# Kernel optimization log

Measured on AMD Instinct MI355X. Metric: run time of the kernel, lower is better.

The kernel has to match this reference:

```python
import jax, jax.numpy as jnp
import numpy as np
from jax import lax
from functools import partial

MAX_FRAMES = 12
NUM_SAMPLES = 500
SIGMA = 0.05
TOPK = 49
LN_EPS = 1e-5


def perturbed_topk_indicators(scores, noise, k):
    """scores: (b, d), noise: (b, ns, d) -> indicators (b, k, d).
    Equivalent to one_hot(sorted_topk_indices).mean(samples) without
    materializing the (b, ns, k, d) one-hot tensor (histogram scatter)."""
    b, ns, d = noise.shape
    perturbed = scores[:, None, :] + SIGMA * noise          # (b, ns, d)
    _, idx = lax.top_k(perturbed, k)                        # (b, ns, k)
    idx = jnp.sort(idx, axis=-1)                            # ascending, as in torch code
    # scatter-add counts into (b, k, d)
    flat = (jnp.arange(b)[:, None, None] * k + jnp.arange(k)[None, None, :]) * d + idx
    counts = jnp.zeros(b * k * d, scores.dtype).at[flat.ravel()].add(1.0)
    return counts.reshape(b, k, d) / ns


def reference(x, ln_w, ln_b, w_in, w_out1, w_out2):
    B, L, D = x.shape
    N = L // MAX_FRAMES
    xf = x.reshape(B * MAX_FRAMES, N, D)                    # (Bf, N, D)
    Bf = B * MAX_FRAMES

    # ---- STPredictorConv ----
    mu = xf.mean(-1, keepdims=True)
    var = jnp.var(xf, axis=-1, keepdims=True)
    xn = (xf - mu) * lax.rsqrt(var + LN_EPS) * ln_w + ln_b
    h = jax.nn.gelu(jnp.einsum('bnd,cd->bnc', xn, w_in), approximate=False)  # (Bf, N, C=256)
    C = h.shape[-1]
    g = h[:, :1, :].reshape(B, MAX_FRAMES, 1, C).mean(axis=1, keepdims=True)  # (B,1,1,C)
    g = jnp.broadcast_to(g, (B, MAX_FRAMES, 1, C)).reshape(Bf, 1, C)
    cat = jnp.concatenate([h, jnp.broadcast_to(g, (Bf, N, C))], axis=-1)      # (Bf, N, 2C)
    s = jax.nn.gelu(jnp.einsum('bnd,cd->bnc', cat, w_out1), approximate=False)
    s = jnp.einsum('bnc,oc->bno', s, w_out2)                # (Bf, N, 1)
    score = jax.nn.softmax(s, axis=-1)[..., 0]              # softmax over size-1 dim -> ones; faithful

    # ---- perturbed top-k selection over spatial tokens ----
    spatial_score = score[:, 1:]                            # (Bf, N-1)
    noise = jax.random.normal(jax.random.key(42), (Bf, NUM_SAMPLES, N - 1), x.dtype)
    ind = perturbed_topk_indicators(spatial_score, noise, TOPK)  # (Bf, k, N-1)

    cls_feat = xf[:, :1, :]
    spatial_feat = xf[:, 1:, :]
    selected = jnp.einsum('bkl,bld->bkd', ind, spatial_feat)
    out = jnp.concatenate([cls_feat, selected], axis=1)     # (Bf, 1+k, D)
    return out.reshape(B, MAX_FRAMES * (1 + TOPK), D)


def setup_inputs() -> dict:
    key = jax.random.key(0)
    ks = jax.random.split(key, 4)
    B, N, D, C = 8, 197, 512, 256
    x = jax.random.normal(ks[0], (B, MAX_FRAMES * N, D), jnp.float32)
    return {
        'x': x,
        'ln_w': jnp.ones((D,), jnp.float32),
        'ln_b': jnp.zeros((D,), jnp.float32),
        'w_in': jax.random.normal(ks[1], (C, D), jnp.float32) * 0.02,
        'w_out1': jax.random.normal(ks[2], (C, D), jnp.float32) * 0.02,
        'w_out2': jax.random.normal(ks[3], (1, C), jnp.float32) * 0.02,
    }
```

## Files before the change

kernel.cpp:

```cpp
#include <hip/hip_runtime.h>
#include <stdint.h>

constexpr int BF   = 96;
constexpr int NS   = 500;
constexpr int DSP  = 196;
constexpr int KSEL = 49;
constexpr int NTOK = 197;
constexpr int DIM  = 512;
constexpr int ROWSTRIDE = 64;

__device__ __forceinline__ uint32_t rotl32(uint32_t x, int r) {
  return __builtin_amdgcn_alignbit(x, x, 32 - r);
}

__device__ __forceinline__ void threefry2x32(uint32_t x0, uint32_t x1,
                                             uint32_t& o0, uint32_t& o1) {
  const uint32_t ks0 = 0u, ks1 = 42u, ks2 = 0u ^ 42u ^ 0x1BD11BDAu;
  x0 += ks0; x1 += ks1;
#define TF_R(r) { x0 += x1; x1 = rotl32(x1, (r)); x1 ^= x0; }
  TF_R(13) TF_R(15) TF_R(26) TF_R(6)   x0 += ks1; x1 += ks2 + 1u;
  TF_R(17) TF_R(29) TF_R(16) TF_R(24)  x0 += ks2; x1 += ks0 + 2u;
  TF_R(13) TF_R(15) TF_R(26) TF_R(6)   x0 += ks0; x1 += ks1 + 3u;
  TF_R(17) TF_R(29) TF_R(16) TF_R(24)  x0 += ks1; x1 += ks2 + 4u;
  TF_R(13) TF_R(15) TF_R(26) TF_R(6)   x0 += ks2; x1 += ks0 + 5u;
#undef TF_R
  o0 = x0; o1 = x1;
}

__device__ __forceinline__ uint32_t noise_bits(uint32_t p) {
  uint32_t o0, o1;
  threefry2x32(0u, p, o0, o1);
  return o0 ^ o1;
}

__global__ __launch_bounds__(256)
void topk_idx_kernel(uint8_t* __restrict__ idxbuf) {
  const int lane = threadIdx.x & 63;
  const int wid  = (blockIdx.x << 2) | (threadIdx.x >> 6);
  const uint32_t rowbase = (uint32_t)wid * (uint32_t)DSP;

  uint32_t m[4];
#pragma unroll
  for (int g = 0; g < 4; ++g) {
    const int j = (g << 6) | lane;
    uint32_t v = 0u;
    if (j < DSP) v = noise_bits(rowbase + (uint32_t)j) >> 9;
    m[g] = v;
  }

  uint32_t T = 0u;
#pragma unroll 1
  for (int bit = 22; bit >= 0; --bit) {
    const uint32_t cand = T | (1u << bit);
    const int c = __popcll(__ballot(m[0] >= cand))
                + __popcll(__ballot(m[1] >= cand))
                + __popcll(__ballot(m[2] >= cand))
                + __popcll(__ballot(m[3] >= cand));
    if (c >= KSEL) T = cand;
  }

  uint64_t gt[4], eq[4];
#pragma unroll
  for (int g = 0; g < 4; ++g) {
    gt[g] = __ballot(m[g] > T);
    eq[g] = __ballot(m[g] == T);
  }
  eq[3] &= 0xFull;

  const int ngt = __popcll(gt[0]) + __popcll(gt[1]) + __popcll(gt[2]) + __popcll(gt[3]);
  const int need = KSEL - ngt;
  const int e0 = __popcll(eq[0]), e1 = __popcll(eq[1]), e2 = __popcll(eq[2]);
  const uint64_t below = (1ull << lane) - 1ull;

  uint64_t fin[4];
  fin[0] = gt[0] | __ballot(((eq[0] >> lane) & 1ull) &&
                            (__popcll(eq[0] & below) < need));
  fin[1] = gt[1] | __ballot(((eq[1] >> lane) & 1ull) &&
                            (e0 + __popcll(eq[1] & below) < need));
  fin[2] = gt[2] | __ballot(((eq[2] >> lane) & 1ull) &&
                            (e0 + e1 + __popcll(eq[2] & below) < need));
  fin[3] = gt[3] | __ballot(((eq[3] >> lane) & 1ull) &&
                            (e0 + e1 + e2 + __popcll(eq[3] & below) < need));

  const int c0 = __popcll(fin[0]);
  const int c1 = c0 + __popcll(fin[1]);
  const int c2 = c1 + __popcll(fin[2]);

  uint8_t* row = idxbuf + (size_t)wid * ROWSTRIDE;
  if ((fin[0] >> lane) & 1ull) row[__popcll(fin[0] & below)]      = (uint8_t)lane;
  if ((fin[1] >> lane) & 1ull) row[c0 + __popcll(fin[1] & below)] = (uint8_t)(64 + lane);
  if ((fin[2] >> lane) & 1ull) row[c1 + __popcll(fin[2] & below)] = (uint8_t)(128 + lane);
  if ((fin[3] >> lane) & 1ull) row[c2 + __popcll(fin[3] & below)] = (uint8_t)(192 + lane);
}

__global__ __launch_bounds__(256)
void hist_kernel(const uint8_t* __restrict__ idxbuf,
                 uint16_t* __restrict__ cnt) {
  const int b = blockIdx.x % BF;
  const int g = blockIdx.x / BF;
  const int t = threadIdx.x;

  __shared__ uint32_t hist[8 * DSP];
  for (int i = t; i < 8 * DSP; i += 256) hist[i] = 0u;
  __syncthreads();

  const uint8_t* base = idxbuf + (size_t)b * NS * ROWSTRIDE + 8 * g;
  for (int r = t; r < NS; r += 256) {
    const uint2 v = *(const uint2*)(base + (size_t)r * ROWSTRIDE);
#pragma unroll
    for (int q = 0; q < 2; ++q) {
      uint32_t w = q ? v.y : v.x;
#pragma unroll
      for (int bb = 0; bb < 4; ++bb) {
        atomicAdd(&hist[(q * 4 + bb) * DSP + (w & 0xffu)], 1u);
        w >>= 8;
      }
    }
  }
  __syncthreads();

  uint16_t* cb = cnt + (size_t)b * KSEL * DSP;
  for (int i = t; i < 8 * DSP; i += 256) {
    const int rank = 8 * g + i / DSP;
    if (rank < KSEL) cb[(size_t)rank * DSP + (i % DSP)] = (uint16_t)hist[i];
  }
}

__global__ __launch_bounds__(256)
void gemm_kernel(const float* __restrict__ x,
                 const uint16_t* __restrict__ cnt,
                 float* __restrict__ out) {
  const int b = blockIdx.x % BF;
  const int tmp = blockIdx.x / BF;
  const int dtile = tmp & 7;
  const int khalf = tmp >> 3;
  const int k0 = khalf * 24;
  const int t = threadIdx.x;
  const int dt = t & 15, kg = t >> 4;

  constexpr int JP = DSP / 2;
  __shared__ uint32_t cfp[32 * JP];
  const uint32_t* cp = (const uint32_t*)(cnt + (size_t)b * KSEL * DSP)
                     + (size_t)k0 * JP;
  for (int i = t; i < 25 * JP; i += 256) cfp[i] = cp[i];
  for (int i = 25 * JP + t; i < 32 * JP; i += 256) cfp[i] = 0u;
  __syncthreads();

  const float* xb = x + (size_t)b * NTOK * DIM + DIM
                  + dtile * 64 + dt * 4;
  float4 acc[2] = {};
#pragma unroll 2
  for (int j2 = 0; j2 < JP; ++j2) {
    const float4 xv0 = *(const float4*)(xb + (size_t)(2 * j2) * DIM);
    const float4 xv1 = *(const float4*)(xb + (size_t)(2 * j2 + 1) * DIM);
#pragma unroll
    for (int i = 0; i < 2; ++i) {
      const uint32_t pr = cfp[(kg + 16 * i) * JP + j2];
      const float c0 = (float)(pr & 0xffffu);
      const float c1 = (float)(pr >> 16);
      acc[i].x = fmaf(c0, xv0.x, acc[i].x);
      acc[i].y = fmaf(c0, xv0.y, acc[i].y);
      acc[i].z = fmaf(c0, xv0.z, acc[i].z);
      acc[i].w = fmaf(c0, xv0.w, acc[i].w);
      acc[i].x = fmaf(c1, xv1.x, acc[i].x);
      acc[i].y = fmaf(c1, xv1.y, acc[i].y);
      acc[i].z = fmaf(c1, xv1.z, acc[i].z);
      acc[i].w = fmaf(c1, xv1.w, acc[i].w);
    }
  }

  float* ob = out + (size_t)b * (1 + KSEL) * DIM + dtile * 64 + dt * 4;
  const float inv = 1.0f / (float)NS;
#pragma unroll
  for (int i = 0; i < 2; ++i) {
    const int kl = kg + 16 * i;
    const int k = k0 + kl;
    if (kl < 25 && k < KSEL) {
      float4 r;
      r.x = acc[i].x * inv; r.y = acc[i].y * inv;
      r.z = acc[i].z * inv; r.w = acc[i].w * inv;
      *(float4*)(ob + (size_t)(1 + k) * DIM) = r;
    }
  }

  if (khalf == 0 && kg == 0) {
    const float4 c4 = *(const float4*)(x + (size_t)b * NTOK * DIM
                                       + dtile * 64 + dt * 4);
    *(float4*)(ob) = c4;
  }
}

extern "C" void kernel_launch(void* const* d_in, const int* in_sizes, int n_in,
                              void* d_out, int out_size, void* d_ws, size_t ws_size,
                              hipStream_t stream) {
  const float* x = (const float*)d_in[0];
  float* out = (float*)d_out;
  uint8_t* idxbuf = (uint8_t*)d_ws;
  uint16_t* cnt = (uint16_t*)((uint8_t*)d_ws +
                              (size_t)BF * NS * ROWSTRIDE);

  topk_idx_kernel<<<dim3(BF * NS / 4), 256, 0, stream>>>(idxbuf);
  hist_kernel<<<dim3(BF * 7), 256, 0, stream>>>(idxbuf, cnt);
  gemm_kernel<<<dim3(BF * 8 * 2), 256, 0, stream>>>(x, cnt, out);
}
```

Baseline: 165.5 us.

## Stage x tiles in LDS and compute all 49 ranks per block in gemm

The gemm kernel no longer splits the 49 ranks into two halves. Each block now computes all ranks for one 64-column tile, which halves the grid and stops x being read twice. Counts are converted to float once into padded shared memory. x is staged through a 32-row LDS tile, with the next tile's global loads issued while the current one is consumed. This adds register pressure, larger LDS use, and a syncthreads-bound loop, and the 49th rank runs on only one thread group.

```diff
diff --git a/kernel.cpp b/kernel.cpp
--- a/kernel.cpp
+++ b/kernel.cpp
@@ -131,59 +131,107 @@
                  const uint16_t* __restrict__ cnt,
                  float* __restrict__ out) {
   const int b = blockIdx.x % BF;
-  const int tmp = blockIdx.x / BF;
-  const int dtile = tmp & 7;
-  const int khalf = tmp >> 3;
-  const int k0 = khalf * 24;
+  const int dtile = blockIdx.x / BF;
   const int t = threadIdx.x;
   const int dt = t & 15, kg = t >> 4;
 
-  constexpr int JP = DSP / 2;
-  __shared__ uint32_t cfp[32 * JP];
-  const uint32_t* cp = (const uint32_t*)(cnt + (size_t)b * KSEL * DSP)
-                     + (size_t)k0 * JP;
-  for (int i = t; i < 25 * JP; i += 256) cfp[i] = cp[i];
-  for (int i = 25 * JP + t; i < 32 * JP; i += 256) cfp[i] = 0u;
-  __syncthreads();
-
-  const float* xb = x + (size_t)b * NTOK * DIM + DIM
-                  + dtile * 64 + dt * 4;
-  float4 acc[2] = {};
-#pragma unroll 2
-  for (int j2 = 0; j2 < JP; ++j2) {
-    const float4 xv0 = *(const float4*)(xb + (size_t)(2 * j2) * DIM);
-    const float4 xv1 = *(const float4*)(xb + (size_t)(2 * j2 + 1) * DIM);
-#pragma unroll
-    for (int i = 0; i < 2; ++i) {
-      const uint32_t pr = cfp[(kg + 16 * i) * JP + j2];
-      const float c0 = (float)(pr & 0xffffu);
-      const float c1 = (float)(pr >> 16);
-      acc[i].x = fmaf(c0, xv0.x, acc[i].x);
-      acc[i].y = fmaf(c0, xv0.y, acc[i].y);
-      acc[i].z = fmaf(c0, xv0.z, acc[i].z);
-      acc[i].w = fmaf(c0, xv0.w, acc[i].w);
-      acc[i].x = fmaf(c1, xv1.x, acc[i].x);
-      acc[i].y = fmaf(c1, xv1.y, acc[i].y);
-      acc[i].z = fmaf(c1, xv1.z, acc[i].z);
-      acc[i].w = fmaf(c1, xv1.w, acc[i].w);
+  constexpr int CFS = 225;
+  __shared__ float cf[KSEL * CFS];
+  __shared__ float xl[32 * 64];
+
+  const uint32_t* cp = (const uint32_t*)(cnt + (size_t)b * KSEL * DSP);
+  for (int i = t; i < KSEL * (DSP / 2); i += 256) {
+    const uint32_t v = cp[i];
+    const int r = i / (DSP / 2), q = i % (DSP / 2);
+    cf[r * CFS + 2 * q]     = (float)(v & 0xffffu);
+    cf[r * CFS + 2 * q + 1] = (float)(v >> 16);
+  }
+  for (int i = t; i < KSEL * (CFS - DSP); i += 256) {
+    const int r = i / (CFS - DSP), q = i % (CFS - DSP);
+    cf[r * CFS + DSP + q] = 0.0f;
+  }
+
+  const float* xsrc = x + (size_t)b * NTOK * DIM + DIM + dtile * 64;
+  const int jl = t >> 3;
+  const int cl = (t & 7) * 8;
+
+  float4 p0, p1;
+  {
+    const float* s = xsrc + (size_t)jl * DIM + cl;
+    p0 = *(const float4*)(s);
+    p1 = *(const float4*)(s + 4);
+  }
+
+  float4 acc[4] = {};
+#pragma unroll 1
+  for (int c = 0; c < 7; ++c) {
+    __syncthreads();
+    {
+      float* d = &xl[jl * 64 + cl];
+      *(float4*)(d) = p0;
+      *(float4*)(d + 4) = p1;
+    }
+    __syncthreads();
+    if (c < 6) {
+      const int nj = 32 * (c + 1);
+      if (c + 1 < 6 || jl < 4) {
+        const float* s = xsrc + (size_t)(nj + jl) * DIM + cl;
+        p0 = *(const float4*)(s);
+        p1 = *(const float4*)(s + 4);
+      }
+    }
+    const int jb = 32 * c;
+#pragma unroll 4
+    for (int j = 0; j < 32; ++j) {
+      const float4 xv = *(const float4*)&xl[j * 64 + dt * 4];
+      const int jc = jb + j;
+      {
+        const float cv = cf[kg * CFS + jc];
+        acc[0].x = fmaf(cv, xv.x, acc[0].x);
+        acc[0].y = fmaf(cv, xv.y, acc[0].y);
+        acc[0].z = fmaf(cv, xv.z, acc[0].z);
+        acc[0].w = fmaf(cv, xv.w, acc[0].w);
+      }
+      {
+        const float cv = cf[(kg + 16) * CFS + jc];
+        acc[1].x = fmaf(cv, xv.x, acc[1].x);
+        acc[1].y = fmaf(cv, xv.y, acc[1].y);
+        acc[1].z = fmaf(cv, xv.z, acc[1].z);
+        acc[1].w = fmaf(cv, xv.w, acc[1].w);
+      }
+      {
+        const float cv = cf[(kg + 32) * CFS + jc];
+        acc[2].x = fmaf(cv, xv.x, acc[2].x);
+        acc[2].y = fmaf(cv, xv.y, acc[2].y);
+        acc[2].z = fmaf(cv, xv.z, acc[2].z);
+        acc[2].w = fmaf(cv, xv.w, acc[2].w);
+      }
+      if (kg == 0) {
+        const float cv = cf[48 * CFS + jc];
+        acc[3].x = fmaf(cv, xv.x, acc[3].x);
+        acc[3].y = fmaf(cv, xv.y, acc[3].y);
+        acc[3].z = fmaf(cv, xv.z, acc[3].z);
+        acc[3].w = fmaf(cv, xv.w, acc[3].w);
+      }
     }
   }
 
   float* ob = out + (size_t)b * (1 + KSEL) * DIM + dtile * 64 + dt * 4;
   const float inv = 1.0f / (float)NS;
-#pragma unroll
-  for (int i = 0; i < 2; ++i) {
-    const int kl = kg + 16 * i;
-    const int k = k0 + kl;
-    if (kl < 25 && k < KSEL) {
-      float4 r;
-      r.x = acc[i].x * inv; r.y = acc[i].y * inv;
-      r.z = acc[i].z * inv; r.w = acc[i].w * inv;
-      *(float4*)(ob + (size_t)(1 + k) * DIM) = r;
-    }
-  }
-
-  if (khalf == 0 && kg == 0) {
+  float4 r;
+  r.x = acc[0].x * inv; r.y = acc[0].y * inv;
+  r.z = acc[0].z * inv; r.w = acc[0].w * inv;
+  *(float4*)(ob + (size_t)(1 + kg) * DIM) = r;
+  r.x = acc[1].x * inv; r.y = acc[1].y * inv;
+  r.z = acc[1].z * inv; r.w = acc[1].w * inv;
+  *(float4*)(ob + (size_t)(1 + kg + 16) * DIM) = r;
+  r.x = acc[2].x * inv; r.y = acc[2].y * inv;
+  r.z = acc[2].z * inv; r.w = acc[2].w * inv;
+  *(float4*)(ob + (size_t)(1 + kg + 32) * DIM) = r;
+  if (kg == 0) {
+    r.x = acc[3].x * inv; r.y = acc[3].y * inv;
+    r.z = acc[3].z * inv; r.w = acc[3].w * inv;
+    *(float4*)(ob + (size_t)(1 + 48) * DIM) = r;
     const float4 c4 = *(const float4*)(x + (size_t)b * NTOK * DIM
                                        + dtile * 64 + dt * 4);
     *(float4*)(ob) = c4;
@@ -201,5 +249,5 @@
 
   topk_idx_kernel<<<dim3(BF * NS / 4), 256, 0, stream>>>(idxbuf);
   hist_kernel<<<dim3(BF * 7), 256, 0, stream>>>(idxbuf, cnt);
-  gemm_kernel<<<dim3(BF * 8 * 2), 256, 0, stream>>>(x, cnt, out);
-}
+  gemm_kernel<<<dim3(BF * 8), 256, 0, stream>>>(x, cnt, out);
+}
```

After: 151.9 us. -8.2%, faster.
